# Kernel optimization log

Measured on AMD Instinct MI355X. Metric: run time of the kernel, lower is better.

The kernel has to match this reference:

```python
import jax, jax.numpy as jnp
import numpy as np

NEG_INF = -9e15  # matches the torch module's zero_vec constant
ALPHA = 0.2      # LeakyReLU negative slope


def setup_inputs() -> dict:
    key = jax.random.key(0)
    k1, k2, k3, k4, k5, k6 = jax.random.split(key, 6)
    N_t, N_o, F_in, F_out = 8192, 8192, 256, 64
    return {
        "t_input": jax.random.normal(k1, (N_t, F_in), dtype=jnp.float32),
        "o_input": jax.random.normal(k2, (N_o, F_in), dtype=jnp.float32),
        "W_t": jax.random.normal(k3, (F_in, F_out), dtype=jnp.float32) * 0.1,
        "W_o": jax.random.normal(k4, (F_in, F_out), dtype=jnp.float32) * 0.1,
        "a": jax.random.normal(k5, (2 * F_out, 1), dtype=jnp.float32) * 0.1,
        "adj": jax.random.randint(k6, (N_t, N_o), 0, 2, dtype=jnp.int32),
    }


def reference(t_input, o_input, W_t, W_o, a, adj):
    # Linear projections
    h_t = t_input @ W_t            # [N_t, F]
    h_o = o_input @ W_o            # [N_o, F]
    F_out = h_t.shape[1]
    a_t = a[:F_out, 0]             # [F]
    a_o = a[F_out:, 0]             # [F]
    # e[i,j] = leakyrelu(cat(h_t[i], h_o[j]) . a) = leakyrelu(h_t[i].a_t + h_o[j].a_o)
    # (avoids materializing the N_t*N_o*2F concat tensor; same math)
    e = jax.nn.leaky_relu(
        (h_t @ a_t)[:, None] + (h_o @ a_o)[None, :], negative_slope=ALPHA
    )                              # [N_t, N_o]
    attention = jnp.where(adj > 0, e, NEG_INF)
    attention = jax.nn.softmax(attention, axis=1)
    # dropout is identity at eval time
    h_prime = attention @ h_o      # [N_t, F]
    return jax.nn.elu(h_prime)     # concat=True
```

## Files before the change

### kernel.cpp

```cpp
#include <hip/hip_runtime.h>
#include <math.h>

#define NT 8192
#define NO 8192
#define FIN 256
#define FOUT 64
#define SPLIT 4
#define JS (NO/SPLIT)
#define ROWT 64
#define TJ 64

#define OFF_ST  ((size_t)0)
#define OFF_SO  (OFF_ST + (size_t)NT)
#define OFF_WT  (OFF_SO + (size_t)NO)
#define OFF_WO  (OFF_WT + (size_t)FIN)
#define OFF_NUM (OFF_WO + (size_t)FIN)
#define OFF_DEN (OFF_NUM + (size_t)SPLIT*NT*FOUT)
#define OFF_HOB (OFF_DEN + (size_t)SPLIT*NT)

typedef __attribute__((ext_vector_type(8))) short short8;
typedef __attribute__((ext_vector_type(4))) float float4v;

static __device__ __forceinline__ unsigned short f2bf(float x) {
  unsigned int u = __float_as_uint(x);
  unsigned int r = (u + 0x7fffu + ((u >> 16) & 1u)) >> 16;
  return (unsigned short)r;
}
static __device__ __forceinline__ float bf2f(unsigned short b) {
  return __uint_as_float(((unsigned int)b) << 16);
}

__global__ void k_wvec(const float* __restrict__ Wt, const float* __restrict__ Wo,
                       const float* __restrict__ a, float* __restrict__ ws) {
  int k = threadIdx.x;
  float s1 = 0.f, s2 = 0.f;
#pragma unroll
  for (int fq = 0; fq < FOUT/4; ++fq) {
    float4 wt4 = *(const float4*)(Wt + (size_t)k*FOUT + fq*4);
    float4 wo4 = *(const float4*)(Wo + (size_t)k*FOUT + fq*4);
    float4 at4 = *(const float4*)(a + fq*4);
    float4 ao4 = *(const float4*)(a + FOUT + fq*4);
    s1 += wt4.x*at4.x + wt4.y*at4.y + wt4.z*at4.z + wt4.w*at4.w;
    s2 += wo4.x*ao4.x + wo4.y*ao4.y + wo4.z*ao4.z + wo4.w*ao4.w;
  }
  ws[OFF_WT + k] = s1;
  ws[OFF_WO + k] = s2;
}

__global__ void k_st(const float* __restrict__ tin, float* __restrict__ ws) {
  int lane = threadIdx.x & 63;
  int wv   = threadIdx.x >> 6;
  int row  = blockIdx.x * 4 + wv;
  float4 v = ((const float4*)(tin + (size_t)row*FIN))[lane];
  float4 w = ((const float4*)(ws + OFF_WT))[lane];
  float p = v.x*w.x + v.y*w.y + v.z*w.z + v.w*w.w;
#pragma unroll
  for (int m = 32; m >= 1; m >>= 1) p += __shfl_xor(p, m, 64);
  if (lane == 0) ws[OFF_ST + row] = p;
}

__global__ void k_ho(const float* __restrict__ oin, const float* __restrict__ Wo,
                     const float* __restrict__ a, float* __restrict__ ws) {
  unsigned short* hob = (unsigned short*)(ws + OFF_HOB);
  int lane = threadIdx.x & 63;
  int wv = __builtin_amdgcn_readfirstlane(threadIdx.x >> 6);
  int r0 = blockIdx.x * 32 + wv * 8;
  const float* ob = oin + (size_t)r0 * FIN;
  float acc[8];
#pragma unroll
  for (int r = 0; r < 8; ++r) acc[r] = 0.f;
#pragma unroll 2
  for (int k = 0; k < FIN; k += 4) {
    float w0 = Wo[(size_t)(k+0)*FOUT + lane];
    float w1 = Wo[(size_t)(k+1)*FOUT + lane];
    float w2 = Wo[(size_t)(k+2)*FOUT + lane];
    float w3 = Wo[(size_t)(k+3)*FOUT + lane];
#pragma unroll
    for (int r = 0; r < 8; ++r) {
      float4 ov = *(const float4*)(ob + (size_t)r*FIN + k);
      acc[r] = fmaf(ov.x, w0, acc[r]);
      acc[r] = fmaf(ov.y, w1, acc[r]);
      acc[r] = fmaf(ov.z, w2, acc[r]);
      acc[r] = fmaf(ov.w, w3, acc[r]);
    }
  }
  float ao = a[FOUT + lane];
#pragma unroll
  for (int r = 0; r < 8; ++r) {
    hob[(size_t)lane*NO + r0 + r] = f2bf(acc[r]);
    float p = acc[r] * ao;
#pragma unroll
    for (int m = 32; m >= 1; m >>= 1) p += __shfl_xor(p, m, 64);
    if (lane == 0) ws[OFF_SO + r0 + r] = p;
  }
}

__launch_bounds__(256, 2)
__global__ void k_attn(const int* __restrict__ adj, float* __restrict__ ws) {
  const float* st = ws + OFF_ST;
  const float* so = ws + OFF_SO;
  const unsigned short* hob = (const unsigned short*)(ws + OFF_HOB);
  float* gnum = ws + OFF_NUM;
  float* gden = ws + OFF_DEN;

  __shared__ float sT[ROWT];
  __shared__ __align__(16) float sO[JS];
  __shared__ __align__(16) unsigned short wB[TJ][72];
  __shared__ __align__(16) unsigned short hB[TJ][72];
  __shared__ float denp[ROWT][16];

  int t  = threadIdx.x;
  int bx = blockIdx.x;
  int s  = bx & (SPLIT - 1);
  int bi = bx >> 2;
  int i0 = bi * ROWT;
  int jbase = s * JS;

  if (t < ROWT) sT[t] = st[i0 + t];
#pragma unroll
  for (int q = 0; q < JS/1024; ++q) {
    int u = q*256 + t;
    ((float4*)sO)[u] = ((const float4*)(so + jbase))[u];
  }
#pragma unroll
  for (int q = 0; q < 4; ++q) ((float*)denp)[q*256 + t] = 0.f;

  int wv = t >> 6, lane = t & 63;
  int iq = (wv >> 1) * 32;
  int fq = (wv & 1) * 32;
  int lm = lane & 15;
  int lk = (lane >> 4) * 8;

  float4v acc[2][2];
#pragma unroll
  for (int mi = 0; mi < 2; ++mi)
#pragma unroll
    for (int fi = 0; fi < 2; ++fi) acc[mi][fi] = (float4v)0.f;

  int hf = t >> 2;
  int hj = (t & 3) * 16;

  for (int tt = 0; tt < JS/TJ; ++tt) {
    int j0 = jbase + tt*TJ;
    __syncthreads();
#pragma unroll
    for (int q = 0; q < 4; ++q) {
      int u = q*256 + t;
      int il = u >> 4, cs = u & 15;
      const int4 av = *(const int4*)(adj + (size_t)(i0 + il)*NO + j0 + cs*4);
      float sti = sT[il];
      int ob = tt*TJ + cs*4;
      float x0 = sti + sO[ob+0]; x0 = fmaxf(x0, 0.2f*x0);
      float x1 = sti + sO[ob+1]; x1 = fmaxf(x1, 0.2f*x1);
      float x2 = sti + sO[ob+2]; x2 = fmaxf(x2, 0.2f*x2);
      float x3 = sti + sO[ob+3]; x3 = fmaxf(x3, 0.2f*x3);
      float w0 = (av.x > 0) ? __expf(x0) : 0.f;
      float w1 = (av.y > 0) ? __expf(x1) : 0.f;
      float w2 = (av.z > 0) ? __expf(x2) : 0.f;
      float w3 = (av.w > 0) ? __expf(x3) : 0.f;
      ushort4 wp;
      wp.x = f2bf(w0); wp.y = f2bf(w1); wp.z = f2bf(w2); wp.w = f2bf(w3);
      *(ushort4*)&wB[il][cs*4] = wp;
      denp[il][cs] += bf2f(wp.x) + bf2f(wp.y) + bf2f(wp.z) + bf2f(wp.w);
    }
    {
      const unsigned short* hg = hob + (size_t)hf*NO + j0 + hj;
      int4 h0 = *(const int4*)(hg);
      int4 h1 = *(const int4*)(hg + 8);
      *(int4*)&hB[hf][hj]     = h0;
      *(int4*)&hB[hf][hj + 8] = h1;
    }
    __syncthreads();
#pragma unroll
    for (int kk = 0; kk < 2; ++kk) {
      short8 a0 = *(const short8*)&wB[iq      + lm][kk*32 + lk];
      short8 a1 = *(const short8*)&wB[iq + 16 + lm][kk*32 + lk];
      short8 b0 = *(const short8*)&hB[fq      + lm][kk*32 + lk];
      short8 b1 = *(const short8*)&hB[fq + 16 + lm][kk*32 + lk];
      acc[0][0] = __builtin_amdgcn_mfma_f32_16x16x32_bf16(a0, b0, acc[0][0], 0, 0, 0);
      acc[0][1] = __builtin_amdgcn_mfma_f32_16x16x32_bf16(a0, b1, acc[0][1], 0, 0, 0);
      acc[1][0] = __builtin_amdgcn_mfma_f32_16x16x32_bf16(a1, b0, acc[1][0], 0, 0, 0);
      acc[1][1] = __builtin_amdgcn_mfma_f32_16x16x32_bf16(a1, b1, acc[1][1], 0, 0, 0);
    }
  }
  __syncthreads();
#pragma unroll
  for (int mi = 0; mi < 2; ++mi)
#pragma unroll
    for (int fi = 0; fi < 2; ++fi)
#pragma unroll
      for (int r = 0; r < 4; ++r) {
        int i = i0 + iq + mi*16 + (lane >> 4)*4 + r;
        int f = fq + fi*16 + lm;
        gnum[((size_t)s*NT + i)*FOUT + f] = acc[mi][fi][r];
      }
  if (t < ROWT) {
    float d = 0.f;
#pragma unroll
    for (int cs = 0; cs < 16; ++cs) d += denp[t][cs];
    gden[(size_t)s*NT + i0 + t] = d;
  }
}

__global__ void k_comb(const float* __restrict__ ws, float* __restrict__ out) {
  int idx = blockIdx.x * 256 + threadIdx.x;
  int i = idx >> 6;
  float num = 0.f, den = 0.f;
#pragma unroll
  for (int s = 0; s < SPLIT; ++s) {
    num += ws[OFF_NUM + ((size_t)s*NT + i)*FOUT + (idx & 63)];
    den += ws[OFF_DEN + (size_t)s*NT + i];
  }
  float r = num / den;
  out[idx] = (r > 0.f) ? r : (__expf(r) - 1.f);
}

extern "C" void kernel_launch(void* const* d_in, const int* in_sizes, int n_in,
                              void* d_out, int out_size, void* d_ws, size_t ws_size,
                              hipStream_t stream) {
  const float* tin = (const float*)d_in[0];
  const float* oin = (const float*)d_in[1];
  const float* Wt  = (const float*)d_in[2];
  const float* Wo  = (const float*)d_in[3];
  const float* a   = (const float*)d_in[4];
  const int*   adj = (const int*)d_in[5];
  float* out = (float*)d_out;
  float* ws  = (float*)d_ws;

  hipLaunchKernelGGL(k_wvec, dim3(1),             dim3(256), 0, stream, Wt, Wo, a, ws);
  hipLaunchKernelGGL(k_st,   dim3(NT/4),          dim3(256), 0, stream, tin, ws);
  hipLaunchKernelGGL(k_ho,   dim3(NO/32),         dim3(256), 0, stream, oin, Wo, a, ws);
  hipLaunchKernelGGL(k_attn, dim3(NT/ROWT*SPLIT), dim3(256), 0, stream, adj, ws);
  hipLaunchKernelGGL(k_comb, dim3(NT*FOUT/256),   dim3(256), 0, stream, ws, out);
}
```

Baseline: 473.7 us.

## Rewrite attention kernel to build MFMA fragments in registers with double-buffered loads

The attention kernel no longer stages weights and h_o tiles through shared memory with block-wide barriers. Each lane now loads its own adjacency, score and h_o fragments straight from global memory into registers, with a two-deep software prefetch. Each wave owns 16 rows across all 64 features. The j-split is raised from 4 to 8 and the launch bounds are raised to 4 blocks per SM, both for more parallelism. In exchange, h_o fragments are reloaded per wave rather than shared within a block, and the combine kernel now sums twice as many partial results.

New measurement: 471.9 us. No clear change (-0.4%).

```diff
diff --git a/kernel.cpp b/kernel.cpp
--- a/kernel.cpp
+++ b/kernel.cpp
@@ -5,10 +5,9 @@
 #define NO 8192
 #define FIN 256
 #define FOUT 64
-#define SPLIT 4
-#define JS (NO/SPLIT)
+#define SPLIT 8
+#define JSP (NO/SPLIT)
 #define ROWT 64
-#define TJ 64
 
 #define OFF_ST  ((size_t)0)
 #define OFF_SO  (OFF_ST + (size_t)NT)
@@ -95,7 +94,7 @@
   }
 }
 
-__launch_bounds__(256, 2)
+__launch_bounds__(256, 4)
 __global__ void k_attn(const int* __restrict__ adj, float* __restrict__ ws) {
   const float* st = ws + OFF_ST;
   const float* so = ws + OFF_SO;
@@ -103,103 +102,85 @@
   float* gnum = ws + OFF_NUM;
   float* gden = ws + OFF_DEN;
 
-  __shared__ float sT[ROWT];
-  __shared__ __align__(16) float sO[JS];
-  __shared__ __align__(16) unsigned short wB[TJ][72];
-  __shared__ __align__(16) unsigned short hB[TJ][72];
-  __shared__ float denp[ROWT][16];
-
-  int t  = threadIdx.x;
+  int t = threadIdx.x;
+  int wv = t >> 6, lane = t & 63;
   int bx = blockIdx.x;
   int s  = bx & (SPLIT - 1);
-  int bi = bx >> 2;
+  int bi = bx >> 3;
   int i0 = bi * ROWT;
-  int jbase = s * JS;
-
-  if (t < ROWT) sT[t] = st[i0 + t];
-#pragma unroll
-  for (int q = 0; q < JS/1024; ++q) {
-    int u = q*256 + t;
-    ((float4*)sO)[u] = ((const float4*)(so + jbase))[u];
-  }
-#pragma unroll
-  for (int q = 0; q < 4; ++q) ((float*)denp)[q*256 + t] = 0.f;
-
-  int wv = t >> 6, lane = t & 63;
-  int iq = (wv >> 1) * 32;
-  int fq = (wv & 1) * 32;
-  int lm = lane & 15;
-  int lk = (lane >> 4) * 8;
-
-  float4v acc[2][2];
-#pragma unroll
-  for (int mi = 0; mi < 2; ++mi)
-#pragma unroll
-    for (int fi = 0; fi < 2; ++fi) acc[mi][fi] = (float4v)0.f;
-
-  int hf = t >> 2;
-  int hj = (t & 3) * 16;
-
-  for (int tt = 0; tt < JS/TJ; ++tt) {
-    int j0 = jbase + tt*TJ;
-    __syncthreads();
-#pragma unroll
-    for (int q = 0; q < 4; ++q) {
-      int u = q*256 + t;
-      int il = u >> 4, cs = u & 15;
-      const int4 av = *(const int4*)(adj + (size_t)(i0 + il)*NO + j0 + cs*4);
-      float sti = sT[il];
-      int ob = tt*TJ + cs*4;
-      float x0 = sti + sO[ob+0]; x0 = fmaxf(x0, 0.2f*x0);
-      float x1 = sti + sO[ob+1]; x1 = fmaxf(x1, 0.2f*x1);
-      float x2 = sti + sO[ob+2]; x2 = fmaxf(x2, 0.2f*x2);
-      float x3 = sti + sO[ob+3]; x3 = fmaxf(x3, 0.2f*x3);
-      float w0 = (av.x > 0) ? __expf(x0) : 0.f;
-      float w1 = (av.y > 0) ? __expf(x1) : 0.f;
-      float w2 = (av.z > 0) ? __expf(x2) : 0.f;
-      float w3 = (av.w > 0) ? __expf(x3) : 0.f;
-      ushort4 wp;
-      wp.x = f2bf(w0); wp.y = f2bf(w1); wp.z = f2bf(w2); wp.w = f2bf(w3);
-      *(ushort4*)&wB[il][cs*4] = wp;
-      denp[il][cs] += bf2f(wp.x) + bf2f(wp.y) + bf2f(wp.z) + bf2f(wp.w);
+  int jb = s * JSP;
+
+  int r16 = lane & 15;
+  int kg  = lane >> 4;
+  int irow = i0 + wv*16 + r16;
+
+  float sti = st[irow];
+
+  const int* ap            = adj + (size_t)irow*NO + jb + kg*8;
+  const float* sop         = so + jb + kg*8;
+  const unsigned short* hp = hob + (size_t)r16*NO + jb + kg*8;
+
+  float4v acc[4];
+#pragma unroll
+  for (int g = 0; g < 4; ++g) acc[g] = (float4v)0.f;
+  float dsum = 0.f;
+
+  int4   A0[2], A1[2];
+  float4 S0[2], S1[2];
+  short8 B[2][4];
+
+  auto load = [&](int buf, int tt) {
+    const int* a = ap + tt*32;
+    A0[buf] = *(const int4*)a;
+    A1[buf] = *(const int4*)(a + 4);
+    const float* sp = sop + tt*32;
+    S0[buf] = *(const float4*)sp;
+    S1[buf] = *(const float4*)(sp + 4);
+#pragma unroll
+    for (int g = 0; g < 4; ++g)
+      B[buf][g] = *(const short8*)(hp + (size_t)g*16*NO + tt*32);
+  };
+
+  auto compute = [&](int buf) {
+    int   m[8] = {A0[buf].x, A0[buf].y, A0[buf].z, A0[buf].w,
+                  A1[buf].x, A1[buf].y, A1[buf].z, A1[buf].w};
+    float v[8] = {S0[buf].x, S0[buf].y, S0[buf].z, S0[buf].w,
+                  S1[buf].x, S1[buf].y, S1[buf].z, S1[buf].w};
+    short8 afrag;
+#pragma unroll
+    for (int e = 0; e < 8; ++e) {
+      float x = sti + v[e];
+      x = fmaxf(x, 0.2f * x);
+      float w = (m[e] > 0) ? __expf(x) : 0.f;
+      unsigned short us = f2bf(w);
+      afrag[e] = (short)us;
+      dsum += bf2f(us);
     }
-    {
-      const unsigned short* hg = hob + (size_t)hf*NO + j0 + hj;
-      int4 h0 = *(const int4*)(hg);
-      int4 h1 = *(const int4*)(hg + 8);
-      *(int4*)&hB[hf][hj]     = h0;
-      *(int4*)&hB[hf][hj + 8] = h1;
+#pragma unroll
+    for (int g = 0; g < 4; ++g)
+      acc[g] = __builtin_amdgcn_mfma_f32_16x16x32_bf16(afrag, B[buf][g], acc[g], 0, 0, 0);
+  };
+
+  load(0, 0);
+#pragma unroll 2
+  for (int tt = 0; tt < JSP/32 - 1; ++tt) {
+    load((tt + 1) & 1, tt + 1);
+    compute(tt & 1);
+  }
+  compute((JSP/32 - 1) & 1);
+
+  dsum += __shfl_xor(dsum, 16, 64);
+  dsum += __shfl_xor(dsum, 32, 64);
+  if (lane < 16) gden[(size_t)s*NT + i0 + wv*16 + lane] = dsum;
+
+#pragma unroll
+  for (int g = 0; g < 4; ++g)
+#pragma unroll
+    for (int r = 0; r < 4; ++r) {
+      int i = i0 + wv*16 + kg*4 + r;
+      int f = g*16 + r16;
+      gnum[((size_t)s*NT + i)*FOUT + f] = acc[g][r];
     }
-    __syncthreads();
-#pragma unroll
-    for (int kk = 0; kk < 2; ++kk) {
-      short8 a0 = *(const short8*)&wB[iq      + lm][kk*32 + lk];
-      short8 a1 = *(const short8*)&wB[iq + 16 + lm][kk*32 + lk];
-      short8 b0 = *(const short8*)&hB[fq      + lm][kk*32 + lk];
-      short8 b1 = *(const short8*)&hB[fq + 16 + lm][kk*32 + lk];
-      acc[0][0] = __builtin_amdgcn_mfma_f32_16x16x32_bf16(a0, b0, acc[0][0], 0, 0, 0);
-      acc[0][1] = __builtin_amdgcn_mfma_f32_16x16x32_bf16(a0, b1, acc[0][1], 0, 0, 0);
-      acc[1][0] = __builtin_amdgcn_mfma_f32_16x16x32_bf16(a1, b0, acc[1][0], 0, 0, 0);
-      acc[1][1] = __builtin_amdgcn_mfma_f32_16x16x32_bf16(a1, b1, acc[1][1], 0, 0, 0);
-    }
-  }
-  __syncthreads();
-#pragma unroll
-  for (int mi = 0; mi < 2; ++mi)
-#pragma unroll
-    for (int fi = 0; fi < 2; ++fi)
-#pragma unroll
-      for (int r = 0; r < 4; ++r) {
-        int i = i0 + iq + mi*16 + (lane >> 4)*4 + r;
-        int f = fq + fi*16 + lm;
-        gnum[((size_t)s*NT + i)*FOUT + f] = acc[mi][fi][r];
-      }
-  if (t < ROWT) {
-    float d = 0.f;
-#pragma unroll
-    for (int cs = 0; cs < 16; ++cs) d += denp[t][cs];
-    gden[(size_t)s*NT + i0 + t] = d;
-  }
 }
 
 __global__ void k_comb(const float* __restrict__ ws, float* __restrict__ out) {
@@ -227,9 +208,9 @@
   float* out = (float*)d_out;
   float* ws  = (float*)d_ws;
 
-  hipLaunchKernelGGL(k_wvec, dim3(1),             dim3(256), 0, stream, Wt, Wo, a, ws);
-  hipLaunchKernelGGL(k_st,   dim3(NT/4),          dim3(256), 0, stream, tin, ws);
-  hipLaunchKernelGGL(k_ho,   dim3(NO/32),         dim3(256), 0, stream, oin, Wo, a, ws);
-  hipLaunchKernelGGL(k_attn, dim3(NT/ROWT*SPLIT), dim3(256), 0, stream, adj, ws);
-  hipLaunchKernelGGL(k_comb, dim3(NT*FOUT/256),   dim3(256), 0, stream, ws, out);
-}
+  hipLaunchKernelGGL(k_wvec, dim3(1),              dim3(256), 0, stream, Wt, Wo, a, ws);
+  hipLaunchKernelGGL(k_st,   dim3(NT/4),           dim3(256), 0, stream, tin, ws);
+  hipLaunchKernelGGL(k_ho,   dim3(NO/32),          dim3(256), 0, stream, oin, Wo, a, ws);
+  hipLaunchKernelGGL(k_attn, dim3(NT/ROWT*SPLIT),  dim3(256), 0, stream, adj, ws);
+  hipLaunchKernelGGL(k_comb, dim3(NT*FOUT/256),    dim3(256), 0, stream, ws, out);
+}
```
